# Kernel tuning notes

Measured on AMD Instinct MI355X. Metric: run time of the kernel, lower is better.

Reference implementation:

```python
import jax, jax.numpy as jnp
import numpy as np

B, H, W, C = 32, 56, 56, 256
HEADS, WS, SS, MLP = 8, 7, 3, 1024
N = WS * WS          # tokens per window = 49
HD = C // HEADS      # head dim = 32
SCALE = HD ** -0.5
EPS = 1e-5


def _rel_pos_index():
    coords = np.stack(np.meshgrid(np.arange(WS), np.arange(WS), indexing='ij')).reshape(2, -1)
    rel = (coords[:, :, None] - coords[:, None, :]).transpose(1, 2, 0)
    rel[:, :, 0] += WS - 1
    rel[:, :, 1] += WS - 1
    rel[:, :, 0] *= 2 * WS - 1
    return rel.sum(-1)  # (49, 49) int


def _shift_mask():
    ma = np.zeros((H, W), np.float32)
    sl = (slice(0, -WS), slice(-WS, -SS), slice(-SS, None))
    cnt = 0
    for hs in sl:
        for ws_ in sl:
            ma[hs, ws_] = cnt
            cnt += 1
    mw = ma.reshape(H // WS, WS, W // WS, WS).transpose(0, 2, 1, 3).reshape(-1, N)
    diff = mw[:, None, :] - mw[:, :, None]
    return np.where(diff != 0, np.float32(-100.0), np.float32(0.0))  # (nW, 49, 49)


_RPI = _rel_pos_index()
_MASK = jnp.asarray(_shift_mask())


def _ln(x, g, b):
    mu = jnp.mean(x, -1, keepdims=True)
    var = jnp.mean(jnp.square(x - mu), -1, keepdims=True)
    return (x - mu) * jax.lax.rsqrt(var + EPS) * g + b


def setup_inputs() -> dict:
    key = jax.random.key(0)
    ks = jax.random.split(key, 6)
    s = 0.02
    return {
        'x': jax.random.normal(ks[0], (B, H * W, C), jnp.float32),
        'qkv_w': jax.random.normal(ks[1], (C, 3 * C), jnp.float32) * s,
        'qkv_b': jnp.zeros((3 * C,), jnp.float32),
        'proj_w': jax.random.normal(ks[2], (C, C), jnp.float32) * s,
        'proj_b': jnp.zeros((C,), jnp.float32),
        'rel_bias': jax.random.normal(ks[3], ((2 * WS - 1) ** 2, HEADS), jnp.float32) * s,
        'ln1_g': jnp.ones((C,), jnp.float32),
        'ln1_b': jnp.zeros((C,), jnp.float32),
        'ln2_g': jnp.ones((C,), jnp.float32),
        'ln2_b': jnp.zeros((C,), jnp.float32),
        'mlp_w1': jax.random.normal(ks[4], (C, MLP), jnp.float32) * s,
        'mlp_b1': jnp.zeros((MLP,), jnp.float32),
        'mlp_w2': jax.random.normal(ks[5], (MLP, C), jnp.float32) * s,
        'mlp_b2': jnp.zeros((C,), jnp.float32),
    }


def reference(x, qkv_w, qkv_b, proj_w, proj_b, rel_bias,
              ln1_g, ln1_b, ln2_g, ln2_b, mlp_w1, mlp_b1, mlp_w2, mlp_b2):
    b = x.shape[0]
    nW = (H // WS) * (W // WS)

    x_skip = x
    xn = _ln(x, ln1_g, ln1_b).reshape(b, H, W, C)
    shifted = jnp.roll(xn, (-SS, -SS), axis=(1, 2))
    # window partition -> (b*nW, N, C)
    xw = shifted.reshape(b, H // WS, WS, W // WS, WS, C)
    xw = xw.transpose(0, 1, 3, 2, 4, 5).reshape(-1, N, C)

    qkv = (xw @ qkv_w + qkv_b).reshape(-1, N, 3, HEADS, HD).transpose(2, 0, 3, 1, 4)
    q, k, v = qkv[0] * SCALE, qkv[1], qkv[2]  # (b*nW, heads, N, hd)

    attn = jnp.einsum('bhnd,bhmd->bhnm', q, k)
    bias = rel_bias[_RPI.reshape(-1)].reshape(N, N, HEADS).transpose(2, 0, 1)
    attn = attn + bias[None]
    attn = attn.reshape(b, nW, HEADS, N, N) + _MASK[None, :, None]
    attn = jax.nn.softmax(attn.reshape(-1, HEADS, N, N), axis=-1)

    out = jnp.einsum('bhnm,bhmd->bhnd', attn, v)
    out = out.transpose(0, 2, 1, 3).reshape(-1, N, C)
    out = out @ proj_w + proj_b

    # window reverse -> (b, H, W, C)
    out = out.reshape(b, H // WS, W // WS, WS, WS, C)
    out = out.transpose(0, 1, 3, 2, 4, 5).reshape(b, H, W, C)
    out = jnp.roll(out, (SS, SS), axis=(1, 2)).reshape(b, H * W, C)

    x = x_skip + out
    x_skip2 = x
    xn2 = _ln(x, ln2_g, ln2_b)
    h = jax.nn.gelu(xn2 @ mlp_w1 + mlp_b1, approximate=False)
    h = h @ mlp_w2 + mlp_b2
    return x_skip2 + h
```

## Files before the change

kernel.cpp:

```cpp
#include <hip/hip_runtime.h>


typedef unsigned short u16;
typedef __attribute__((ext_vector_type(8))) short bfrag8;
typedef __attribute__((ext_vector_type(8))) unsigned short u16x8;
typedef __attribute__((ext_vector_type(4))) float f32x4;

#define WS_TOK 49
#define C_DIM 256
#define M_ROWS 100352
#define N_WIN 2048
#define SCALE_Q 0.17677669529663689f

#if defined(__has_builtin)
#  if __has_builtin(__builtin_amdgcn_global_load_lds)
#    define HAVE_GLL 1
#  endif
#endif
#ifndef HAVE_GLL
#  define HAVE_GLL 0
#endif

__device__ __forceinline__ float u2f(u16 u) {
    union { unsigned int i; float f; } c; c.i = ((unsigned int)u) << 16; return c.f;
}
__device__ __forceinline__ u16 f2u(float f) {
    union { float f; unsigned int i; } c; c.f = f;
    unsigned int i = c.i;
    return (u16)((i + 0x7fffu + ((i >> 16) & 1u)) >> 16);
}
__device__ __forceinline__ int regionOf(int h) {
    return h < 49 ? 0 : (h < 53 ? 1 : 2);
}
__device__ __forceinline__ float gelu_tanh(float v) {
    const float y = 0.79788456080286536f * (v + 0.044715f * v * v * v);
    const float e = __expf(2.f * y);
    const float t = 1.f - 2.f / (e + 1.f);
    return 0.5f * v * (1.f + t);
}

__device__ __forceinline__ void g2l16(const u16* g, u16* l) {
#if HAVE_GLL
    __builtin_amdgcn_global_load_lds((const __attribute__((address_space(1))) void*)g,
                                     (__attribute__((address_space(3))) void*)l, 16, 0, 0);
#else
    *(bfrag8*)l = *(const bfrag8*)g;
#endif
}

__global__ void transpose_k(const float* __restrict__ in, u16* __restrict__ out,
                            int R, int Ccols) {
    int i = blockIdx.x * 256 + threadIdx.x;
    if (i < R * Ccols) {
        int r = i / Ccols, c = i - r * Ccols;
        out[(size_t)c * R + r] = f2u(in[i]);
    }
}

__global__ __launch_bounds__(256) void ln_kernel(const float* __restrict__ xin,
                                                 const float* __restrict__ g,
                                                 const float* __restrict__ b,
                                                 u16* __restrict__ out, int mode) {
    const int w = threadIdx.x >> 6, lane = threadIdx.x & 63;
    const int r = blockIdx.x * 4 + w;
    int s = r;
    if (mode == 0) {
        const int win = r / WS_TOK, tok = r - win * WS_TOK;
        const int b_ = win >> 6, w64 = win & 63;
        const int wr = w64 >> 3, wc = w64 & 7;
        const int th = tok / 7, tw = tok - th * 7;
        int hh = wr * 7 + th + 3; if (hh >= 56) hh -= 56;
        int ww = wc * 7 + tw + 3; if (ww >= 56) ww -= 56;
        s = b_ * 3136 + hh * 56 + ww;
    }
    const float4 u = *(const float4*)(xin + (size_t)s * C_DIM + lane * 4);
    float f0 = u.x, f1 = u.y, f2 = u.z, f3 = u.w;
    float s1 = f0 + f1 + f2 + f3;
    float s2 = f0 * f0 + f1 * f1 + f2 * f2 + f3 * f3;
#pragma unroll
    for (int off = 32; off; off >>= 1) {
        s1 += __shfl_xor(s1, off, 64);
        s2 += __shfl_xor(s2, off, 64);
    }
    const float mu = s1 * (1.f / 256.f);
    const float rs = rsqrtf(s2 * (1.f / 256.f) - mu * mu + 1e-5f);
    const float4 ug = *(const float4*)(g + lane * 4);
    const float4 ub = *(const float4*)(b + lane * 4);
    ushort4 o;
    o.x = f2u((f0 - mu) * rs * ug.x + ub.x);
    o.y = f2u((f1 - mu) * rs * ug.y + ub.y);
    o.z = f2u((f2 - mu) * rs * ug.z + ub.z);
    o.w = f2u((f3 - mu) * rs * ug.w + ub.w);
    *(ushort4*)(out + (size_t)r * C_DIM + lane * 4) = o;
}

template <int KD, int ND, int NY, int EPI>
__global__ __launch_bounds__(256) void gemm_bt(const u16* __restrict__ A,
                                               const u16* __restrict__ Bt,
                                               const float* __restrict__ bias,
                                               u16* __restrict__ o0,
                                               u16* __restrict__ o1,
                                               u16* __restrict__ o2,
                                               float* __restrict__ fo,
                                               const float* __restrict__ res) {
    __shared__ __align__(16) char pool[32768];
    u16* As = (u16*)pool;
    u16* Bs = (u16*)(pool + 16384);
    const int tid = threadIdx.x;
    const int bid = blockIdx.x;
    const int m0 = (bid / NY) * 128;
    const int n0 = (bid % NY) * 128;
    const int wid = tid >> 6, lane = tid & 63;
    const int wy = wid >> 1, wx = wid & 1;
    const int l15 = lane & 15, lsel = lane >> 4;

    f32x4 acc[4][4] = {};
    const u16* Ag = A + (size_t)m0 * KD;
    const u16* Bg = Bt + (size_t)n0 * KD;

    for (int k0 = 0; k0 < KD; k0 += 64) {
#pragma unroll
        for (int p = 0; p < 4; ++p) {
            const int idx = p * 256 + tid;
            const int row = idx >> 3, s = idx & 7;
            const int so = (s ^ (row & 7)) << 3;
            g2l16(Ag + (size_t)row * KD + k0 + so, As + idx * 8);
            g2l16(Bg + (size_t)row * KD + k0 + so, Bs + idx * 8);
        }
        __syncthreads();
#pragma unroll
        for (int kh = 0; kh < 2; ++kh) {
            bfrag8 af[4], bfv[4];
#pragma unroll
            for (int m = 0; m < 4; ++m) {
                const int r = wy * 64 + m * 16 + l15;
                af[m] = *(const bfrag8*)(As + r * 64 +
                         ((kh * 32 + lsel * 8) ^ ((r & 7) << 3)));
            }
#pragma unroll
            for (int n = 0; n < 4; ++n) {
                const int r = wx * 64 + n * 16 + l15;
                bfv[n] = *(const bfrag8*)(Bs + r * 64 +
                          ((kh * 32 + lsel * 8) ^ ((r & 7) << 3)));
            }
#pragma unroll
            for (int m = 0; m < 4; ++m)
#pragma unroll
                for (int n = 0; n < 4; ++n)
                    acc[m][n] = __builtin_amdgcn_mfma_f32_16x16x32_bf16(
                        af[m], bfv[n], acc[m][n], 0, 0, 0);
        }
        __syncthreads();
    }

    float* Ts = (float*)pool + wid * (16 * 68);
    const int r  = lane >> 2;
    const int cg = (lane & 3) << 4;

#pragma unroll
    for (int m = 0; m < 4; ++m) {
#pragma unroll
        for (int n = 0; n < 4; ++n)
#pragma unroll
            for (int reg = 0; reg < 4; ++reg)
                Ts[(lsel * 4 + reg) * 68 + n * 16 + l15] = acc[m][n][reg];
        float vals[16];
#pragma unroll
        for (int j = 0; j < 4; ++j)
            *(f32x4*)(vals + 4 * j) = *(const f32x4*)(Ts + r * 68 + cg + 4 * j);

        const int gr  = m0 + wy * 64 + m * 16 + r;
        const int gc0 = n0 + wx * 64 + cg;
        float bias16[16];
#pragma unroll
        for (int j = 0; j < 4; ++j)
            *(f32x4*)(bias16 + 4 * j) = *(const f32x4*)(bias + gc0 + 4 * j);

        if (EPI == 0) {
            const int win = gr / WS_TOK, tok = gr - win * WS_TOK;
            const int part = gc0 >> 8, head = (gc0 >> 5) & 7, hd = gc0 & 31;
            u16* dst = (part == 0) ? o0 : (part == 1) ? o1 : o2;
            const float sc = (part == 0) ? SCALE_Q : 1.f;
            const size_t di = (size_t)win * 8 * (WS_TOK * 32) + (size_t)tok * 32 +
                              (size_t)head * (WS_TOK * 32) + hd;
            u16x8 pk[2];
#pragma unroll
            for (int j = 0; j < 16; ++j)
                ((u16*)pk)[j] = f2u((vals[j] + bias16[j]) * sc);
            *(u16x8*)(dst + di)     = pk[0];
            *(u16x8*)(dst + di + 8) = pk[1];
        } else if (EPI == 1) {
            const int win = gr / WS_TOK, tok = gr - win * WS_TOK;
            const int b_ = win >> 6, w64 = win & 63;
            const int wr = w64 >> 3, wc = w64 & 7;
            const int th = tok / 7, tw = tok - th * 7;
            int hh = wr * 7 + th + 3; if (hh >= 56) hh -= 56;
            int ww = wc * 7 + tw + 3; if (ww >= 56) ww -= 56;
            const size_t di = ((size_t)b_ * 3136 + hh * 56 + ww) * C_DIM + gc0;
#pragma unroll
            for (int j = 0; j < 4; ++j) {
                f32x4 rr = *(const f32x4*)(res + di + 4 * j);
                f32x4 o;
#pragma unroll
                for (int e = 0; e < 4; ++e)
                    o[e] = rr[e] + vals[4 * j + e] + bias16[4 * j + e];
                *(f32x4*)(fo + di + 4 * j) = o;
            }
        } else if (EPI == 2) {
            u16x8 pk[2];
#pragma unroll
            for (int j = 0; j < 16; ++j)
                ((u16*)pk)[j] = f2u(gelu_tanh(vals[j] + bias16[j]));
            u16* dst = o0 + (size_t)gr * ND + gc0;
            *(u16x8*)dst       = pk[0];
            *(u16x8*)(dst + 8) = pk[1];
        } else {
            const size_t di = (size_t)gr * ND + gc0;
#pragma unroll
            for (int j = 0; j < 4; ++j) {
                f32x4 rr = *(const f32x4*)(res + di + 4 * j);
                f32x4 o;
#pragma unroll
                for (int e = 0; e < 4; ++e)
                    o[e] = rr[e] + vals[4 * j + e] + bias16[4 * j + e];
                *(f32x4*)(fo + di + 4 * j) = o;
            }
        }
    }
}

__device__ __forceinline__ void stage_w1t(const u16* __restrict__ w1T, u16* dst,
                                          int kc, int k0, int tid) {
#pragma unroll
    for (int p = 0; p < 4; ++p) {
        const int i = p * 256 + tid;
        const int row = i >> 3, s = i & 7;
        g2l16(w1T + (size_t)(kc * 128 + row) * 256 + k0 + ((s ^ (row & 7)) << 3),
              dst + i * 8);
    }
}
__device__ __forceinline__ void stage_w2t(const u16* __restrict__ w2T, u16* dst,
                                          int kc, int bs, int tid) {
#pragma unroll
    for (int p = 0; p < 4; ++p) {
        const int i = p * 256 + tid;
        const int row = i >> 2, s = i & 3;
        g2l16(w2T + (size_t)row * 1024 + kc * 128 + bs * 32 +
                  ((s ^ ((row >> 1) & 3)) << 3),
              dst + i * 8);
    }
}

__global__ __launch_bounds__(256, 2) void fused_mlp(const u16* __restrict__ z,
                                                    const u16* __restrict__ w1T,
                                                    const float* __restrict__ b1,
                                                    const u16* __restrict__ w2T,
                                                    const float* __restrict__ b2,
                                                    float* __restrict__ out) {
    __shared__ __align__(16) u16 pool[40960];
    u16* zS  = pool;
    u16* wb0 = pool + 16384;
    u16* wb1 = pool + 24576;
    u16* hc  = pool + 32768;
    const int tid = threadIdx.x;
    const int wid = tid >> 6, lane = tid & 63;
    const int wy = wid >> 1, wx = wid & 1;
    const int l15 = lane & 15, lsel = lane >> 4;
    const int m0 = blockIdx.x * 64;

#pragma unroll
    for (int p = 0; p < 8; ++p) {
        const int i = p * 256 + tid;
        const int row = i >> 5, s = i & 31;
        g2l16(z + (size_t)(m0 + row) * 256 + ((s ^ (row & 7)) << 3), zS + i * 8);
    }
    stage_w1t(w1T, wb0, 0, 0, tid);
    __syncthreads();

    f32x4 acc2[2][8] = {};

    for (int kc = 0; kc < 8; ++kc) {
        float b1v[4];
#pragma unroll
        for (int n = 0; n < 4; ++n)
            b1v[n] = b1[kc * 128 + wx * 64 + n * 16 + l15];

        f32x4 acc1[2][4] = {};
#pragma unroll
        for (int ks = 0; ks < 4; ++ks) {
            u16* wc = (ks & 1) ? wb1 : wb0;
            u16* wn = (ks & 1) ? wb0 : wb1;
            if (ks < 3) stage_w1t(w1T, wn, kc, (ks + 1) * 64, tid);
            else        stage_w2t(w2T, wn, kc, 0, tid);
#pragma unroll
            for (int sub = 0; sub < 2; ++sub) {
                bfrag8 af[2], bf[4];
#pragma unroll
                for (int m = 0; m < 2; ++m) {
                    const int r = wy * 32 + m * 16 + l15;
                    af[m] = *(const bfrag8*)(zS + r * 256 +
                             ((ks * 64 + sub * 32 + lsel * 8) ^ ((r & 7) << 3)));
                }
#pragma unroll
                for (int n = 0; n < 4; ++n) {
                    const int r = wx * 64 + n * 16 + l15;
                    bf[n] = *(const bfrag8*)(wc + r * 64 +
                             ((sub * 32 + lsel * 8) ^ ((r & 7) << 3)));
                }
#pragma unroll
                for (int m = 0; m < 2; ++m)
#pragma unroll
                    for (int n = 0; n < 4; ++n)
                        acc1[m][n] = __builtin_amdgcn_mfma_f32_16x16x32_bf16(
                            af[m], bf[n], acc1[m][n], 0, 0, 0);
            }
            if (ks == 3) {
#pragma unroll
                for (int m = 0; m < 2; ++m)
#pragma unroll
                    for (int n = 0; n < 4; ++n)
#pragma unroll
                        for (int reg = 0; reg < 4; ++reg) {
                            const int rh = wy * 32 + m * 16 + lsel * 4 + reg;
                            const int ch = wx * 64 + n * 16 + l15;
                            hc[rh * 128 + (ch ^ ((rh & 15) << 3))] =
                                f2u(gelu_tanh(acc1[m][n][reg] + b1v[n]));
                        }
            }
            __syncthreads();
        }
#pragma unroll
        for (int bs = 0; bs < 4; ++bs) {
            u16* wc = (bs & 1) ? wb1 : wb0;
            u16* wn = (bs & 1) ? wb0 : wb1;
            if (bs < 3)      stage_w2t(w2T, wn, kc, bs + 1, tid);
            else if (kc < 7) stage_w1t(w1T, wn, kc + 1, 0, tid);
            bfrag8 a2[2], bb[8];
#pragma unroll
            for (int m = 0; m < 2; ++m) {
                const int r = wy * 32 + m * 16 + l15;
                a2[m] = *(const bfrag8*)(hc + r * 128 +
                         ((bs * 32 + lsel * 8) ^ ((r & 15) << 3)));
            }
#pragma unroll
            for (int n = 0; n < 8; ++n) {
                const int r = wx * 128 + n * 16 + l15;
                bb[n] = *(const bfrag8*)(wc + r * 32 +
                         ((lsel * 8) ^ (((r >> 1) & 3) << 3)));
            }
#pragma unroll
            for (int m = 0; m < 2; ++m)
#pragma unroll
                for (int n = 0; n < 8; ++n)
                    acc2[m][n] = __builtin_amdgcn_mfma_f32_16x16x32_bf16(
                        a2[m], bb[n], acc2[m][n], 0, 0, 0);
            __syncthreads();
        }
    }

    float b2v[8];
#pragma unroll
    for (int n = 0; n < 8; ++n)
        b2v[n] = b2[wx * 128 + n * 16 + l15];
#pragma unroll
    for (int m = 0; m < 2; ++m)
#pragma unroll
        for (int reg = 0; reg < 4; ++reg) {
            const int row = m0 + wy * 32 + m * 16 + lsel * 4 + reg;
#pragma unroll
            for (int n = 0; n < 8; ++n) {
                const size_t di = (size_t)row * 256 + wx * 128 + n * 16 + l15;
                out[di] += acc2[m][n][reg] + b2v[n];
            }
        }
}

__global__ __launch_bounds__(256) void attn_kernel(const u16* __restrict__ q,
                                                   const u16* __restrict__ k,
                                                   const u16* __restrict__ v,
                                                   const float* __restrict__ relb,
                                                   u16* __restrict__ ao) {
    __shared__ __align__(16) u16 PbAll[4][64 * 64];
    __shared__ __align__(16) u16 VtAll[4][32 * 64];
    const int wid = threadIdx.x >> 6;
    const int lane = threadIdx.x & 63;
    u16* Pb = PbAll[wid];
    u16* Vt = VtAll[wid];
    const int bid = blockIdx.x * 4 + wid;
    const int head = bid & 7, win = bid >> 3;
    const int w64 = win & 63;
    const int wr = w64 >> 3, wc = w64 & 7;
    const int l15 = lane & 15, lsel = lane >> 4;
    const size_t base = (size_t)bid * (WS_TOK * 32);
    const u16* qb = q + base;
    const u16* kb = k + base;
    const u16* vb = v + base;

    for (int idx = lane; idx < WS_TOK * 32; idx += 64) {
        const int tok = idx >> 5, dim = idx & 31;
        Vt[dim * 64 + (tok ^ ((dim & 7) << 3))] = vb[idx];
    }
    for (int i = lane; i < 32 * 15; i += 64) {
        const int dim = i / 15, tok = 49 + (i - dim * 15);
        Vt[dim * 64 + (tok ^ ((dim & 7) << 3))] = 0;
    }

    bfrag8 qf[4], kf[4];
#pragma unroll
    for (int m = 0; m < 4; ++m) {
        int tok = m * 16 + l15; if (tok > 48) tok = 48;
        qf[m] = *(const bfrag8*)(qb + tok * 32 + lsel * 8);
    }
#pragma unroll
    for (int n = 0; n < 4; ++n) {
        int tok = n * 16 + l15; if (tok > 48) tok = 48;
        kf[n] = *(const bfrag8*)(kb + tok * 32 + lsel * 8);
    }
    f32x4 S[4][4] = {};
#pragma unroll
    for (int m = 0; m < 4; ++m)
#pragma unroll
        for (int n = 0; n < 4; ++n)
            S[m][n] = __builtin_amdgcn_mfma_f32_16x16x32_bf16(qf[m], kf[n], S[m][n], 0, 0, 0);

#pragma unroll
    for (int m = 0; m < 4; ++m) {
#pragma unroll
        for (int reg = 0; reg < 4; ++reg) {
            const int row = m * 16 + lsel * 4 + reg;
            const int rowc = row > 48 ? 48 : row;
            const int ih = rowc / 7, iw = rowc - ih * 7;
            const int ri = regionOf(wr * 7 + ih) * 3 + regionOf(wc * 7 + iw);
            float sv[4];
#pragma unroll
            for (int n = 0; n < 4; ++n) {
                const int col = n * 16 + l15;
                float val = S[m][n][reg];
                if (col > 48) {
                    val = -1e30f;
                } else {
                    const int jh = col / 7, jw = col - jh * 7;
                    val += relb[((ih - jh + 6) * 13 + (iw - jw + 6)) * 8 + head];
                    const int rj = regionOf(wr * 7 + jh) * 3 + regionOf(wc * 7 + jw);
                    if (ri != rj) val -= 100.f;
                }
                sv[n] = val;
            }
            float mx = fmaxf(fmaxf(sv[0], sv[1]), fmaxf(sv[2], sv[3]));
#pragma unroll
            for (int off = 1; off < 16; off <<= 1) mx = fmaxf(mx, __shfl_xor(mx, off, 64));
            float p[4], sum = 0.f;
#pragma unroll
            for (int n = 0; n < 4; ++n) { p[n] = __expf(sv[n] - mx); sum += p[n]; }
#pragma unroll
            for (int off = 1; off < 16; off <<= 1) sum += __shfl_xor(sum, off, 64);
            const float inv = 1.f / sum;
#pragma unroll
            for (int n = 0; n < 4; ++n)
                Pb[row * 64 + ((n * 16 + l15) ^ ((row & 7) << 3))] = f2u(p[n] * inv);
        }
    }

    f32x4 O[4][2] = {};
    bfrag8 vf[2][2];
#pragma unroll
    for (int n = 0; n < 2; ++n) {
        const int r = n * 16 + l15;
        vf[n][0] = *(const bfrag8*)(Vt + r * 64 + ((lsel * 8) ^ ((r & 7) << 3)));
        vf[n][1] = *(const bfrag8*)(Vt + r * 64 + ((32 + lsel * 8) ^ ((r & 7) << 3)));
    }
#pragma unroll
    for (int m = 0; m < 4; ++m) {
        const int r = m * 16 + l15;
        const bfrag8 pf0 = *(const bfrag8*)(Pb + r * 64 +
                            ((lsel * 8) ^ ((r & 7) << 3)));
        const bfrag8 pf1 = *(const bfrag8*)(Pb + r * 64 +
                            ((32 + lsel * 8) ^ ((r & 7) << 3)));
#pragma unroll
        for (int n = 0; n < 2; ++n) {
            O[m][n] = __builtin_amdgcn_mfma_f32_16x16x32_bf16(pf0, vf[n][0], O[m][n], 0, 0, 0);
            O[m][n] = __builtin_amdgcn_mfma_f32_16x16x32_bf16(pf1, vf[n][1], O[m][n], 0, 0, 0);
        }
    }
    const size_t aob = (size_t)win * (WS_TOK * C_DIM) + head * 32;
#pragma unroll
    for (int m = 0; m < 4; ++m) {
#pragma unroll
        for (int reg = 0; reg < 4; ++reg) {
            const int row = m * 16 + lsel * 4 + reg;
            if (row < WS_TOK) {
#pragma unroll
                for (int n = 0; n < 2; ++n)
                    ao[aob + (size_t)row * C_DIM + n * 16 + l15] = f2u(O[m][n][reg]);
            }
        }
    }
}

extern "C" void kernel_launch(void* const* d_in, const int* in_sizes, int n_in,
                              void* d_out, int out_size, void* d_ws, size_t ws_size,
                              hipStream_t stream) {
    (void)in_sizes; (void)n_in; (void)out_size; (void)ws_size;
    const float* x      = (const float*)d_in[0];
    const float* qkv_w  = (const float*)d_in[1];
    const float* qkv_b  = (const float*)d_in[2];
    const float* proj_w = (const float*)d_in[3];
    const float* proj_b = (const float*)d_in[4];
    const float* relb   = (const float*)d_in[5];
    const float* ln1g   = (const float*)d_in[6];
    const float* ln1b   = (const float*)d_in[7];
    const float* ln2g   = (const float*)d_in[8];
    const float* ln2b   = (const float*)d_in[9];
    const float* w1     = (const float*)d_in[10];
    const float* b1     = (const float*)d_in[11];
    const float* w2     = (const float*)d_in[12];
    const float* b2     = (const float*)d_in[13];
    float* out = (float*)d_out;

    const size_t SZ = (size_t)M_ROWS * C_DIM;
    u16* wsu  = (u16*)d_ws;
    u16* xw   = wsu;
    u16* qq   = wsu + SZ;
    u16* kk   = wsu + 2 * SZ;
    u16* vv   = wsu + 3 * SZ;
    u16* ao   = wsu + 4 * SZ;
    u16* z    = xw;
    u16* qkvT = wsu + 5 * SZ;
    u16* projT = qkvT + 256 * 768;
    u16* w1T  = projT + 256 * 256;
    u16* w2T  = w1T + 256 * 1024;

    transpose_k<<<768, 256, 0, stream>>>(qkv_w, qkvT, 256, 768);
    transpose_k<<<256, 256, 0, stream>>>(proj_w, projT, 256, 256);
    transpose_k<<<1024, 256, 0, stream>>>(w1, w1T, 256, 1024);
    transpose_k<<<1024, 256, 0, stream>>>(w2, w2T, 1024, 256);

    ln_kernel<<<M_ROWS / 4, 256, 0, stream>>>(x, ln1g, ln1b, xw, 0);

    gemm_bt<256, 768, 6, 0><<<784 * 6, 256, 0, stream>>>(xw, qkvT, qkv_b,
                                                         qq, kk, vv, nullptr, nullptr);

    attn_kernel<<<N_WIN * 8 / 4, 256, 0, stream>>>(qq, kk, vv, relb, ao);

    gemm_bt<256, 256, 2, 1><<<784 * 2, 256, 0, stream>>>(ao, projT, proj_b,
                                                         nullptr, nullptr, nullptr, out, x);

    ln_kernel<<<M_ROWS / 4, 256, 0, stream>>>(out, ln2g, ln2b, z, 1);

    fused_mlp<<<M_ROWS / 64, 256, 0, stream>>>(z, w1T, b1, w2T, b2, out);
}
```

Baseline: 674.2 us.

## Fuse projection GEMM with residual add and second LayerNorm

Replaces the generic projection GEMM plus separate LN2 kernel with one kernel. Each block computes a full 256-column row tile, adds bias and residual, and computes LayerNorm statistics via shuffles and shared-memory partials. It writes both the fp32 residual output and the bf16 normalized input for the MLP. The four weight transpose launches are also merged into one. This removes a full read/write pass over the activation tensor, at the cost of fewer, larger blocks and extra block-wide syncs in the epilogue.

```diff
diff --git a/kernel.cpp b/kernel.cpp
--- a/kernel.cpp
+++ b/kernel.cpp
@@ -48,12 +48,22 @@
 #endif
 }
 
-__global__ void transpose_k(const float* __restrict__ in, u16* __restrict__ out,
-                            int R, int Ccols) {
-    int i = blockIdx.x * 256 + threadIdx.x;
+__global__ void transpose_all(const float* __restrict__ qkv_w,
+                              const float* __restrict__ proj_w,
+                              const float* __restrict__ w1,
+                              const float* __restrict__ w2,
+                              u16* __restrict__ qkvT, u16* __restrict__ projT,
+                              u16* __restrict__ w1T, u16* __restrict__ w2T) {
+    const int bid = blockIdx.x;
+    const float* in; u16* outp; int R, Ccols, base;
+    if (bid < 768)       { in = qkv_w;  outp = qkvT;  R = 256;  Ccols = 768;  base = bid; }
+    else if (bid < 1024) { in = proj_w; outp = projT; R = 256;  Ccols = 256;  base = bid - 768; }
+    else if (bid < 2048) { in = w1;     outp = w1T;   R = 256;  Ccols = 1024; base = bid - 1024; }
+    else                 { in = w2;     outp = w2T;   R = 1024; Ccols = 256;  base = bid - 2048; }
+    const int i = base * 256 + threadIdx.x;
     if (i < R * Ccols) {
-        int r = i / Ccols, c = i - r * Ccols;
-        out[(size_t)c * R + r] = f2u(in[i]);
+        const int r = i / Ccols, c = i - r * Ccols;
+        outp[(size_t)c * R + r] = f2u(in[i]);
     }
 }
 
@@ -189,43 +199,138 @@
                 ((u16*)pk)[j] = f2u((vals[j] + bias16[j]) * sc);
             *(u16x8*)(dst + di)     = pk[0];
             *(u16x8*)(dst + di + 8) = pk[1];
-        } else if (EPI == 1) {
-            const int win = gr / WS_TOK, tok = gr - win * WS_TOK;
-            const int b_ = win >> 6, w64 = win & 63;
-            const int wr = w64 >> 3, wc = w64 & 7;
-            const int th = tok / 7, tw = tok - th * 7;
-            int hh = wr * 7 + th + 3; if (hh >= 56) hh -= 56;
-            int ww = wc * 7 + tw + 3; if (ww >= 56) ww -= 56;
-            const size_t di = ((size_t)b_ * 3136 + hh * 56 + ww) * C_DIM + gc0;
-#pragma unroll
-            for (int j = 0; j < 4; ++j) {
-                f32x4 rr = *(const f32x4*)(res + di + 4 * j);
-                f32x4 o;
-#pragma unroll
-                for (int e = 0; e < 4; ++e)
-                    o[e] = rr[e] + vals[4 * j + e] + bias16[4 * j + e];
-                *(f32x4*)(fo + di + 4 * j) = o;
-            }
-        } else if (EPI == 2) {
-            u16x8 pk[2];
-#pragma unroll
-            for (int j = 0; j < 16; ++j)
-                ((u16*)pk)[j] = f2u(gelu_tanh(vals[j] + bias16[j]));
-            u16* dst = o0 + (size_t)gr * ND + gc0;
-            *(u16x8*)dst       = pk[0];
-            *(u16x8*)(dst + 8) = pk[1];
-        } else {
-            const size_t di = (size_t)gr * ND + gc0;
-#pragma unroll
-            for (int j = 0; j < 4; ++j) {
-                f32x4 rr = *(const f32x4*)(res + di + 4 * j);
-                f32x4 o;
-#pragma unroll
-                for (int e = 0; e < 4; ++e)
-                    o[e] = rr[e] + vals[4 * j + e] + bias16[4 * j + e];
-                *(f32x4*)(fo + di + 4 * j) = o;
-            }
-        }
+        }
+    }
+}
+
+__global__ __launch_bounds__(256, 2) void proj_ln(const u16* __restrict__ A,
+                                                  const u16* __restrict__ Bt,
+                                                  const float* __restrict__ bias,
+                                                  const float* __restrict__ res,
+                                                  const float* __restrict__ g2,
+                                                  const float* __restrict__ b2,
+                                                  float* __restrict__ out,
+                                                  u16* __restrict__ zout) {
+    __shared__ __align__(16) char pool[49152];
+    u16* As = (u16*)pool;
+    u16* Bs = (u16*)(pool + 16384);
+    const int tid = threadIdx.x;
+    const int m0 = blockIdx.x * 128;
+    const int wid = tid >> 6, lane = tid & 63;
+    const int wy = wid >> 1, wx = wid & 1;
+    const int l15 = lane & 15, lsel = lane >> 4;
+
+    f32x4 acc[4][8] = {};
+    const u16* Ag = A + (size_t)m0 * 256;
+
+    for (int k0 = 0; k0 < 256; k0 += 64) {
+#pragma unroll
+        for (int p = 0; p < 4; ++p) {
+            const int idx = p * 256 + tid;
+            const int row = idx >> 3, s = idx & 7;
+            g2l16(Ag + (size_t)row * 256 + k0 + ((s ^ (row & 7)) << 3),
+                  As + idx * 8);
+        }
+#pragma unroll
+        for (int p = 0; p < 8; ++p) {
+            const int idx = p * 256 + tid;
+            const int row = idx >> 3, s = idx & 7;
+            g2l16(Bt + (size_t)row * 256 + k0 + ((s ^ (row & 7)) << 3),
+                  Bs + idx * 8);
+        }
+        __syncthreads();
+#pragma unroll
+        for (int kh = 0; kh < 2; ++kh) {
+            bfrag8 af[4], bf[8];
+#pragma unroll
+            for (int m = 0; m < 4; ++m) {
+                const int r = wy * 64 + m * 16 + l15;
+                af[m] = *(const bfrag8*)(As + r * 64 +
+                         ((kh * 32 + lsel * 8) ^ ((r & 7) << 3)));
+            }
+#pragma unroll
+            for (int n = 0; n < 8; ++n) {
+                const int r = wx * 128 + n * 16 + l15;
+                bf[n] = *(const bfrag8*)(Bs + r * 64 +
+                         ((kh * 32 + lsel * 8) ^ ((r & 7) << 3)));
+            }
+#pragma unroll
+            for (int m = 0; m < 4; ++m)
+#pragma unroll
+                for (int n = 0; n < 8; ++n)
+                    acc[m][n] = __builtin_amdgcn_mfma_f32_16x16x32_bf16(
+                        af[m], bf[n], acc[m][n], 0, 0, 0);
+        }
+        __syncthreads();
+    }
+
+    float* Ts = (float*)pool + wid * (16 * 132);
+    float* part = (float*)(pool + 33792);
+    const int r4 = lane >> 2;
+    const int cg = (lane & 3) << 5;
+
+#pragma unroll
+    for (int m = 0; m < 4; ++m) {
+#pragma unroll
+        for (int n = 0; n < 8; ++n)
+#pragma unroll
+            for (int reg = 0; reg < 4; ++reg)
+                Ts[(lsel * 4 + reg) * 132 + n * 16 + l15] = acc[m][n][reg];
+        float vals[32];
+#pragma unroll
+        for (int j = 0; j < 8; ++j)
+            *(f32x4*)(vals + 4 * j) = *(const f32x4*)(Ts + r4 * 132 + cg + 4 * j);
+
+        const int gr  = m0 + wy * 64 + m * 16 + r4;
+        const int gc0 = wx * 128 + cg;
+        const int win = gr / WS_TOK, tok = gr - win * WS_TOK;
+        const int b_ = win >> 6, w64 = win & 63;
+        const int wr = w64 >> 3, wc = w64 & 7;
+        const int th = tok / 7, tw = tok - th * 7;
+        int hh = wr * 7 + th + 3; if (hh >= 56) hh -= 56;
+        int ww = wc * 7 + tw + 3; if (ww >= 56) ww -= 56;
+        const size_t rowbase = ((size_t)b_ * 3136 + hh * 56 + ww) * C_DIM;
+
+        float s1 = 0.f, s2 = 0.f;
+#pragma unroll
+        for (int j = 0; j < 8; ++j) {
+            f32x4 rr = *(const f32x4*)(res + rowbase + gc0 + 4 * j);
+            f32x4 b4 = *(const f32x4*)(bias + gc0 + 4 * j);
+#pragma unroll
+            for (int e = 0; e < 4; ++e) {
+                const float v = rr[e] + vals[4 * j + e] + b4[e];
+                vals[4 * j + e] = v;
+                s1 += v; s2 += v * v;
+            }
+        }
+        s1 += __shfl_xor(s1, 1, 64); s2 += __shfl_xor(s2, 1, 64);
+        s1 += __shfl_xor(s1, 2, 64); s2 += __shfl_xor(s2, 2, 64);
+        const int prow = wy * 64 + m * 16 + r4;
+        if ((lane & 3) == 0) {
+            part[(prow * 2 + wx) * 2 + 0] = s1;
+            part[(prow * 2 + wx) * 2 + 1] = s2;
+        }
+        __syncthreads();
+        const float t1 = part[(prow * 2 + 0) * 2 + 0] + part[(prow * 2 + 1) * 2 + 0];
+        const float t2 = part[(prow * 2 + 0) * 2 + 1] + part[(prow * 2 + 1) * 2 + 1];
+        const float mu = t1 * (1.f / 256.f);
+        const float rs = rsqrtf(t2 * (1.f / 256.f) - mu * mu + 1e-5f);
+        u16x8 pk[4];
+#pragma unroll
+        for (int j = 0; j < 8; ++j) {
+            f32x4 v = *(const f32x4*)(vals + 4 * j);
+            *(f32x4*)(out + rowbase + gc0 + 4 * j) = v;
+            f32x4 gg = *(const f32x4*)(g2 + gc0 + 4 * j);
+            f32x4 bb = *(const f32x4*)(b2 + gc0 + 4 * j);
+#pragma unroll
+            for (int e = 0; e < 4; ++e)
+                ((u16*)pk)[4 * j + e] = f2u((v[e] - mu) * rs * gg[e] + bb[e]);
+        }
+        u16* zd = zout + rowbase + gc0;
+#pragma unroll
+        for (int j = 0; j < 4; ++j)
+            *(u16x8*)(zd + 8 * j) = pk[j];
+        __syncthreads();
     }
 }
 
@@ -530,10 +635,8 @@
     u16* w1T  = projT + 256 * 256;
     u16* w2T  = w1T + 256 * 1024;
 
-    transpose_k<<<768, 256, 0, stream>>>(qkv_w, qkvT, 256, 768);
-    transpose_k<<<256, 256, 0, stream>>>(proj_w, projT, 256, 256);
-    transpose_k<<<1024, 256, 0, stream>>>(w1, w1T, 256, 1024);
-    transpose_k<<<1024, 256, 0, stream>>>(w2, w2T, 1024, 256);
+    transpose_all<<<3072, 256, 0, stream>>>(qkv_w, proj_w, w1, w2,
+                                            qkvT, projT, w1T, w2T);
 
     ln_kernel<<<M_ROWS / 4, 256, 0, stream>>>(x, ln1g, ln1b, xw, 0);
 
@@ -542,10 +645,7 @@
 
     attn_kernel<<<N_WIN * 8 / 4, 256, 0, stream>>>(qq, kk, vv, relb, ao);
 
-    gemm_bt<256, 256, 2, 1><<<784 * 2, 256, 0, stream>>>(ao, projT, proj_b,
-                                                         nullptr, nullptr, nullptr, out, x);
-
-    ln_kernel<<<M_ROWS / 4, 256, 0, stream>>>(out, ln2g, ln2b, z, 1);
+    proj_ln<<<784, 256, 0, stream>>>(ao, projT, proj_b, x, ln2g, ln2b, out, z);
 
     fused_mlp<<<M_ROWS / 64, 256, 0, stream>>>(z, w1T, b1, w2T, b2, out);
 }
```

Result: slower. 703.3 us (+4.3%).
